# Kernel tuning notes

Hardware: AMD Instinct MI355X
Metric: run time of the kernel (lower is better)

## Reference

```python
import jax, jax.numpy as jnp
import numpy as np

B, C, L = 8, 512, 2048
D = C // 8  # qk projection dim


def setup_inputs() -> dict:
    key = jax.random.key(0)
    ks = jax.random.split(key, 7)
    s = 0.02
    return {
        "x": jax.random.normal(ks[0], (B, C, L), dtype=jnp.float32),
        "data_mask": jnp.zeros((B, L, L), dtype=bool),
        "Wq": jax.random.normal(ks[1], (D, C), dtype=jnp.float32) * s,
        "bq": jnp.zeros((D,), dtype=jnp.float32),
        "Wk": jax.random.normal(ks[2], (D, C), dtype=jnp.float32) * s,
        "bk": jnp.zeros((D,), dtype=jnp.float32),
        "Wv": jax.random.normal(ks[3], (C, C), dtype=jnp.float32) * s,
        "bv": jnp.zeros((C,), dtype=jnp.float32),
    }


def reference(x, data_mask, Wq, bq, Wk, bk, Wv, bv):
    # Conv1d(kernel_size=1) == pointwise linear over channel dim.
    Lx = x.shape[-1]
    q = jnp.einsum("dc,bcl->bld", Wq, x) + bq              # (B, L, D)  == query_conv(x).permute(0,2,1)
    k = jnp.einsum("dc,bcl->bdl", Wk, x) + bk[:, None]     # (B, D, L)
    energy = jnp.einsum("bld,bdm->blm", q, k)              # (B, L, L)
    causal = jnp.triu(jnp.ones((Lx, Lx), dtype=bool), k=1)  # strictly-upper = masked
    mask = causal[None, :, :] | data_mask
    energy = jnp.where(mask, -jnp.inf, energy)
    attention = jax.nn.softmax(energy, axis=-1)            # (B, L, L)
    v = jnp.einsum("oc,bcl->bol", Wv, x) + bv[:, None]     # (B, C, L)
    # out = bmm(proj_value, attention^T): out[b,c,m] = sum_l v[b,c,l] * attention[b,m,l]
    out = jnp.einsum("bcl,bml->bcm", v, attention)         # (B, C, L)
    return out, attention
```

## Files before the change

### kernel.cpp

```cpp
#include <hip/hip_runtime.h>
#include <cstddef>
#include <math.h>

#define B_ 8
#define C_ 512
#define L_ 2048
#define D_ 64

typedef __bf16 bf16x8 __attribute__((ext_vector_type(8)));
typedef __bf16 bf16x4 __attribute__((ext_vector_type(4)));
typedef float f32x4 __attribute__((ext_vector_type(4)));

__device__ __forceinline__ void async_lds16(const void* g, void* l) {
  __builtin_amdgcn_global_load_lds(
      (const __attribute__((address_space(1))) void*)g,
      (__attribute__((address_space(3))) void*)l, 16, 0, 0);
}

__global__ __launch_bounds__(256) void transpose_cvt(const float* __restrict__ x,
                                                     __bf16* __restrict__ xT) {
  __shared__ float t[32][33];
  const int b = blockIdx.z;
  const int l0 = blockIdx.x * 32, c0 = blockIdx.y * 32;
  const int tx = threadIdx.x & 31, ty = threadIdx.x >> 5;
  const float* xb = x + (size_t)b * C_ * L_;
#pragma unroll
  for (int r = 0; r < 4; ++r)
    t[ty + r * 8][tx] = xb[(size_t)(c0 + ty + r * 8) * L_ + l0 + tx];
  __syncthreads();
  __bf16* xTb = xT + (size_t)b * L_ * C_;
#pragma unroll
  for (int r = 0; r < 4; ++r)
    xTb[(size_t)(l0 + ty + r * 8) * C_ + c0 + tx] = (__bf16)t[tx][ty + r * 8];
}

__global__ __launch_bounds__(256) void cvt_bf16(const float* __restrict__ in,
                                                __bf16* __restrict__ out, int n4) {
  const int i = blockIdx.x * 256 + threadIdx.x;
  if (i < n4) {
    float4 v = ((const float4*)in)[i];
    bf16x4 h = {(__bf16)v.x, (__bf16)v.y, (__bf16)v.z, (__bf16)v.w};
    ((bf16x4*)out)[i] = h;
  }
}

template <int TRANS>
__global__ __launch_bounds__(256) void proj_gemm(
    const float* __restrict__ W, const float* __restrict__ bias,
    const float* __restrict__ x, __bf16* __restrict__ out, int M) {
  __shared__ float As[16][68];
  __shared__ float Bs[16][68];
  const int b = blockIdx.z;
  const int m0 = blockIdx.x * 64;
  const int n0 = blockIdx.y * 64;
  const float* xb = x + (size_t)b * C_ * L_;
  const int tid = threadIdx.x;
  const int tm = tid >> 4, tn = tid & 15;
  const int la_m = tid >> 2, la_k = (tid & 3) * 4;
  const int lb_k = tid >> 4, lb_n = (tid & 15) * 4;
  float acc[4][4] = {};
  for (int k0 = 0; k0 < C_; k0 += 16) {
    float4 a4 = *(const float4*)(W + (size_t)(m0 + la_m) * C_ + k0 + la_k);
    As[la_k + 0][la_m] = a4.x;
    As[la_k + 1][la_m] = a4.y;
    As[la_k + 2][la_m] = a4.z;
    As[la_k + 3][la_m] = a4.w;
    float4 b4 = *(const float4*)(xb + (size_t)(k0 + lb_k) * L_ + n0 + lb_n);
    *(float4*)&Bs[lb_k][lb_n] = b4;
    __syncthreads();
#pragma unroll
    for (int k = 0; k < 16; ++k) {
      float4 av = *(const float4*)&As[k][tm * 4];
      float4 bv = *(const float4*)&Bs[k][tn * 4];
      float a[4] = {av.x, av.y, av.z, av.w};
      float bb[4] = {bv.x, bv.y, bv.z, bv.w};
#pragma unroll
      for (int i = 0; i < 4; ++i)
#pragma unroll
        for (int j = 0; j < 4; ++j) acc[i][j] = fmaf(a[i], bb[j], acc[i][j]);
    }
    __syncthreads();
  }
#pragma unroll
  for (int i = 0; i < 4; ++i) {
    const int c = m0 + tm * 4 + i;
    const float bi = bias[c];
#pragma unroll
    for (int j = 0; j < 4; ++j) {
      const int l = n0 + tn * 4 + j;
      const float vv = acc[i][j] + bi;
      if (TRANS)
        out[((size_t)b * L_ + l) * D_ + c] = (__bf16)vv;
      else
        out[((size_t)b * M + c) * L_ + l] = (__bf16)vv;
    }
  }
}

__global__ __launch_bounds__(256) void energy_softmax(
    const __bf16* __restrict__ q, const __bf16* __restrict__ k,
    const unsigned char* __restrict__ mask, float* __restrict__ att) {
  __shared__ __align__(16) __bf16 qs[32 * 64];
  __shared__ __align__(16) __bf16 ks[2][128 * 64];
  __shared__ __align__(16) unsigned char msk[2][32 * 128];
  __shared__ float sums[4][32];
  __shared__ float invs[32];
  const int b = blockIdx.y;
  const int tid = threadIdx.x;
  const int w = tid >> 6, lane = tid & 63;
  const int lm = lane & 15, q8 = lane >> 4;
  const __bf16* qb = q + (size_t)b * L_ * D_;
  const __bf16* kb = k + (size_t)b * L_ * D_;

  for (int half = 0; half < 2; ++half) {
    const int s = half ? (63 - (int)blockIdx.x) : (int)blockIdx.x;
    const int r0 = s * 32;
    const int T = (r0 + 31) / 128 + 1;
    bf16x8 af[2][2];
    float inv[2][4];

    for (int pass = 0; pass < 2; ++pass) {
      __syncthreads();
      if (pass == 0)
        async_lds16(qb + (size_t)r0 * D_ + tid * 8, &qs[w * 512]);
#pragma unroll
      for (int r = 0; r < 4; ++r)
        async_lds16(kb + (size_t)(r * 32) * D_ + tid * 8,
                    &ks[0][r * 2048 + w * 512]);
      async_lds16(mask + (size_t)((size_t)b * L_ + r0 + w * 8 + (lane >> 3)) * L_ +
                      (lane & 7) * 16,
                  &msk[0][w * 1024]);

      float rsum[2][4] = {};
      for (int t = 0; t < T; ++t) {
        const int t0 = t * 128;
        const int buf = t & 1;
        __syncthreads();
        if (pass == 0 && t == 0) {
#pragma unroll
          for (int i = 0; i < 2; ++i)
#pragma unroll
            for (int kk = 0; kk < 2; ++kk)
              af[i][kk] =
                  *(const bf16x8*)&qs[(i * 16 + lm) * 64 + kk * 32 + q8 * 8];
        }
        if (t + 1 < T) {
          const int nt0 = t0 + 128, nb = (t + 1) & 1;
#pragma unroll
          for (int r = 0; r < 4; ++r)
            async_lds16(kb + (size_t)(nt0 + r * 32) * D_ + tid * 8,
                        &ks[nb][r * 2048 + w * 512]);
          async_lds16(mask +
                          (size_t)((size_t)b * L_ + r0 + w * 8 + (lane >> 3)) * L_ +
                          nt0 + (lane & 7) * 16,
                      &msk[nb][w * 1024]);
        }
        f32x4 acc[2][2] = {};
#pragma unroll
        for (int kk = 0; kk < 2; ++kk) {
#pragma unroll
          for (int j = 0; j < 2; ++j) {
            bf16x8 bf = *(const bf16x8*)&ks[buf][(w * 32 + j * 16 + lm) * 64 +
                                                 kk * 32 + q8 * 8];
#pragma unroll
            for (int i = 0; i < 2; ++i)
              acc[i][j] = __builtin_amdgcn_mfma_f32_16x16x32_bf16(
                  af[i][kk], bf, acc[i][j], 0, 0, 0);
          }
        }
#pragma unroll
        for (int i = 0; i < 2; ++i) {
#pragma unroll
          for (int j = 0; j < 2; ++j) {
#pragma unroll
            for (int r = 0; r < 4; ++r) {
              const int lr = i * 16 + q8 * 4 + r;
              const int mcol = w * 32 + j * 16 + lm;
              const int l = r0 + lr, m = t0 + mcol;
              const bool ok = (m <= l) && (msk[buf][lr * 128 + mcol] == 0);
              const float p = ok ? __expf(acc[i][j][r]) : 0.f;
              if (pass == 0)
                rsum[i][r] += p;
              else
                att[((size_t)b * L_ + l) * L_ + m] = p * inv[i][r];
            }
          }
        }
      }
      if (pass == 0) {
#pragma unroll
        for (int i = 0; i < 2; ++i)
#pragma unroll
          for (int r = 0; r < 4; ++r) {
            float v = rsum[i][r];
            v += __shfl_xor(v, 1);
            v += __shfl_xor(v, 2);
            v += __shfl_xor(v, 4);
            v += __shfl_xor(v, 8);
            if (lm == 0) sums[w][i * 16 + q8 * 4 + r] = v;
          }
        __syncthreads();
        if (tid < 32)
          invs[tid] =
              1.f / (sums[0][tid] + sums[1][tid] + sums[2][tid] + sums[3][tid]);
        __syncthreads();
#pragma unroll
        for (int i = 0; i < 2; ++i)
#pragma unroll
          for (int r = 0; r < 4; ++r) inv[i][r] = invs[i * 16 + q8 * 4 + r];
      }
    }
    const float4 z4 = {0.f, 0.f, 0.f, 0.f};
    for (int rr = 0; rr < 32; ++rr) {
      float* arow = att + ((size_t)b * L_ + r0 + rr) * L_;
      for (int c = T * 128 + tid * 4; c < L_; c += 1024)
        *(float4*)&arow[c] = z4;
    }
  }
}

template <int B_CVT, int OUT_BF16, int HAS_BIAS, int TRUNC>
__global__ __launch_bounds__(256) void gemm_bt_mfma(
    const __bf16* __restrict__ A, const void* __restrict__ Bmat,
    const float* __restrict__ bias, void* __restrict__ Cout, int N, int K,
    int lda, int ldb, size_t strideA, size_t strideB, size_t strideC) {
  __shared__ __align__(16) __bf16 Ash[128 * 32];
  __shared__ __align__(16) __bf16 Bsh[128 * 32];
  const int b = blockIdx.z;
  const int m0 = blockIdx.x * 128;
  const int n0 = blockIdx.y * 128;
  const int tid = threadIdx.x;
  const int w = tid >> 6, lane = tid & 63;
  const int wm = (w & 1) * 64, wn = (w >> 1) * 64;
  const int lm = lane & 15, q8 = lane >> 4;

  const __bf16* Ab = A + strideA * b;
  const __bf16* Bh = (const __bf16*)Bmat + strideB * b;
  const float* Bf = (const float*)Bmat + strideB * b;

  f32x4 acc[4][4] = {};
  const int kmax = TRUNC ? (n0 + 128) : K;

  for (int k0 = 0; k0 < kmax; k0 += 32) {
#pragma unroll
    for (int t = 0; t < 2; ++t) {
      const int row_base = (t * 4 + w) * 16;
      const int row = row_base + (lane >> 2);
      const int k8 = lane & 3;
      async_lds16(Ab + (size_t)(m0 + row) * lda + k0 + k8 * 8,
                  &Ash[row_base * 32]);
    }
    if (B_CVT) {
#pragma unroll
      for (int t = 0; t < 4; ++t) {
        const int linear = t * 256 + tid;
        const int row = linear >> 3, k4 = linear & 7;
        float4 v4 = *(const float4*)(Bf + (size_t)(n0 + row) * ldb + k0 + k4 * 4);
        bf16x4 h = {(__bf16)v4.x, (__bf16)v4.y, (__bf16)v4.z, (__bf16)v4.w};
        *(bf16x4*)&Bsh[row * 32 + k4 * 4] = h;
      }
    } else {
#pragma unroll
      for (int t = 0; t < 2; ++t) {
        const int row_base = (t * 4 + w) * 16;
        const int row = row_base + (lane >> 2);
        const int k8 = lane & 3;
        async_lds16(Bh + (size_t)(n0 + row) * ldb + k0 + k8 * 8,
                    &Bsh[row_base * 32]);
      }
    }
    __syncthreads();
    bf16x8 af[4], bfr[4];
#pragma unroll
    for (int i = 0; i < 4; ++i) {
      af[i] = *(const bf16x8*)&Ash[(wm + i * 16 + lm) * 32 + q8 * 8];
      bfr[i] = *(const bf16x8*)&Bsh[(wn + i * 16 + lm) * 32 + q8 * 8];
    }
#pragma unroll
    for (int i = 0; i < 4; ++i)
#pragma unroll
      for (int j = 0; j < 4; ++j)
        acc[i][j] = __builtin_amdgcn_mfma_f32_16x16x32_bf16(af[i], bfr[j],
                                                            acc[i][j], 0, 0, 0);
    __syncthreads();
  }

#pragma unroll
  for (int i = 0; i < 4; ++i) {
#pragma unroll
    for (int j = 0; j < 4; ++j) {
      const int ng = n0 + wn + j * 16 + lm;
#pragma unroll
      for (int r = 0; r < 4; ++r) {
        const int mg = m0 + wm + i * 16 + q8 * 4 + r;
        float val = acc[i][j][r];
        if (HAS_BIAS) val += bias[mg];
        if (OUT_BF16)
          ((__bf16*)Cout)[strideC * b + (size_t)mg * N + ng] = (__bf16)val;
        else
          ((float*)Cout)[strideC * b + (size_t)mg * N + ng] = val;
      }
    }
  }
}

extern "C" void kernel_launch(void* const* d_in, const int* in_sizes, int n_in,
                              void* d_out, int out_size, void* d_ws,
                              size_t ws_size, hipStream_t stream) {
  const float* x = (const float*)d_in[0];
  const unsigned char* dmask = (const unsigned char*)d_in[1];
  const float* Wq = (const float*)d_in[2];
  const float* bq = (const float*)d_in[3];
  const float* Wk = (const float*)d_in[4];
  const float* bk = (const float*)d_in[5];
  const float* Wv = (const float*)d_in[6];
  const float* bv = (const float*)d_in[7];

  float* out = (float*)d_out;
  float* att = out + (size_t)B_ * C_ * L_;

  __bf16* qh = (__bf16*)d_ws;
  __bf16* kh = qh + (size_t)B_ * L_ * D_;
  __bf16* xTh = kh + (size_t)B_ * L_ * D_;
  __bf16* Wvh = xTh + (size_t)B_ * L_ * C_;
  __bf16* vh = Wvh + (size_t)C_ * C_;

  dim3 blk(256);
  transpose_cvt<<<dim3(L_ / 32, C_ / 32, B_), blk, 0, stream>>>(x, xTh);
  cvt_bf16<<<dim3((C_ * C_ / 4 + 255) / 256), blk, 0, stream>>>(Wv, Wvh,
                                                                C_ * C_ / 4);
  proj_gemm<1><<<dim3(1, 32, B_), blk, 0, stream>>>(Wq, bq, x, qh, D_);
  proj_gemm<1><<<dim3(1, 32, B_), blk, 0, stream>>>(Wk, bk, x, kh, D_);
  gemm_bt_mfma<0, 1, 1, 0><<<dim3(C_ / 128, L_ / 128, B_), blk, 0, stream>>>(
      Wvh, xTh, bv, vh, L_, C_, C_, C_, 0, (size_t)L_ * C_, (size_t)C_ * L_);
  energy_softmax<<<dim3(32, B_), blk, 0, stream>>>(qh, kh, dmask, att);
  gemm_bt_mfma<1, 0, 0, 1><<<dim3(C_ / 128, L_ / 128, B_), blk, 0, stream>>>(
      vh, att, nullptr, out, L_, L_, L_, L_, (size_t)C_ * L_, (size_t)L_ * L_,
      (size_t)C_ * L_);
}
```

Baseline: 477.4 us.

## Fuse attention-value product into softmax kernel and use MFMA for Q/K projection

Measured after the change: 418.1 us. 1.14x faster.

```diff
diff --git a/kernel.cpp b/kernel.cpp
--- a/kernel.cpp
+++ b/kernel.cpp
@@ -10,6 +10,8 @@
 typedef __bf16 bf16x8 __attribute__((ext_vector_type(8)));
 typedef __bf16 bf16x4 __attribute__((ext_vector_type(4)));
 typedef float f32x4 __attribute__((ext_vector_type(4)));
+
+#define MFMA16 __builtin_amdgcn_mfma_f32_16x16x32_bf16
 
 __device__ __forceinline__ void async_lds16(const void* g, void* l) {
   __builtin_amdgcn_global_load_lds(
@@ -44,186 +46,28 @@
   }
 }
 
-template <int TRANS>
-__global__ __launch_bounds__(256) void proj_gemm(
-    const float* __restrict__ W, const float* __restrict__ bias,
-    const float* __restrict__ x, __bf16* __restrict__ out, int M) {
-  __shared__ float As[16][68];
-  __shared__ float Bs[16][68];
-  const int b = blockIdx.z;
-  const int m0 = blockIdx.x * 64;
-  const int n0 = blockIdx.y * 64;
-  const float* xb = x + (size_t)b * C_ * L_;
-  const int tid = threadIdx.x;
-  const int tm = tid >> 4, tn = tid & 15;
-  const int la_m = tid >> 2, la_k = (tid & 3) * 4;
-  const int lb_k = tid >> 4, lb_n = (tid & 15) * 4;
-  float acc[4][4] = {};
-  for (int k0 = 0; k0 < C_; k0 += 16) {
-    float4 a4 = *(const float4*)(W + (size_t)(m0 + la_m) * C_ + k0 + la_k);
-    As[la_k + 0][la_m] = a4.x;
-    As[la_k + 1][la_m] = a4.y;
-    As[la_k + 2][la_m] = a4.z;
-    As[la_k + 3][la_m] = a4.w;
-    float4 b4 = *(const float4*)(xb + (size_t)(k0 + lb_k) * L_ + n0 + lb_n);
-    *(float4*)&Bs[lb_k][lb_n] = b4;
-    __syncthreads();
-#pragma unroll
-    for (int k = 0; k < 16; ++k) {
-      float4 av = *(const float4*)&As[k][tm * 4];
-      float4 bv = *(const float4*)&Bs[k][tn * 4];
-      float a[4] = {av.x, av.y, av.z, av.w};
-      float bb[4] = {bv.x, bv.y, bv.z, bv.w};
-#pragma unroll
-      for (int i = 0; i < 4; ++i)
-#pragma unroll
-        for (int j = 0; j < 4; ++j) acc[i][j] = fmaf(a[i], bb[j], acc[i][j]);
-    }
-    __syncthreads();
-  }
-#pragma unroll
-  for (int i = 0; i < 4; ++i) {
-    const int c = m0 + tm * 4 + i;
-    const float bi = bias[c];
-#pragma unroll
-    for (int j = 0; j < 4; ++j) {
-      const int l = n0 + tn * 4 + j;
-      const float vv = acc[i][j] + bi;
-      if (TRANS)
-        out[((size_t)b * L_ + l) * D_ + c] = (__bf16)vv;
-      else
-        out[((size_t)b * M + c) * L_ + l] = (__bf16)vv;
-    }
-  }
-}
-
-__global__ __launch_bounds__(256) void energy_softmax(
-    const __bf16* __restrict__ q, const __bf16* __restrict__ k,
-    const unsigned char* __restrict__ mask, float* __restrict__ att) {
-  __shared__ __align__(16) __bf16 qs[32 * 64];
-  __shared__ __align__(16) __bf16 ks[2][128 * 64];
-  __shared__ __align__(16) unsigned char msk[2][32 * 128];
-  __shared__ float sums[4][32];
-  __shared__ float invs[32];
-  const int b = blockIdx.y;
-  const int tid = threadIdx.x;
-  const int w = tid >> 6, lane = tid & 63;
-  const int lm = lane & 15, q8 = lane >> 4;
-  const __bf16* qb = q + (size_t)b * L_ * D_;
-  const __bf16* kb = k + (size_t)b * L_ * D_;
-
-  for (int half = 0; half < 2; ++half) {
-    const int s = half ? (63 - (int)blockIdx.x) : (int)blockIdx.x;
-    const int r0 = s * 32;
-    const int T = (r0 + 31) / 128 + 1;
-    bf16x8 af[2][2];
-    float inv[2][4];
-
-    for (int pass = 0; pass < 2; ++pass) {
-      __syncthreads();
-      if (pass == 0)
-        async_lds16(qb + (size_t)r0 * D_ + tid * 8, &qs[w * 512]);
-#pragma unroll
-      for (int r = 0; r < 4; ++r)
-        async_lds16(kb + (size_t)(r * 32) * D_ + tid * 8,
-                    &ks[0][r * 2048 + w * 512]);
-      async_lds16(mask + (size_t)((size_t)b * L_ + r0 + w * 8 + (lane >> 3)) * L_ +
-                      (lane & 7) * 16,
-                  &msk[0][w * 1024]);
-
-      float rsum[2][4] = {};
-      for (int t = 0; t < T; ++t) {
-        const int t0 = t * 128;
-        const int buf = t & 1;
-        __syncthreads();
-        if (pass == 0 && t == 0) {
-#pragma unroll
-          for (int i = 0; i < 2; ++i)
-#pragma unroll
-            for (int kk = 0; kk < 2; ++kk)
-              af[i][kk] =
-                  *(const bf16x8*)&qs[(i * 16 + lm) * 64 + kk * 32 + q8 * 8];
-        }
-        if (t + 1 < T) {
-          const int nt0 = t0 + 128, nb = (t + 1) & 1;
-#pragma unroll
-          for (int r = 0; r < 4; ++r)
-            async_lds16(kb + (size_t)(nt0 + r * 32) * D_ + tid * 8,
-                        &ks[nb][r * 2048 + w * 512]);
-          async_lds16(mask +
-                          (size_t)((size_t)b * L_ + r0 + w * 8 + (lane >> 3)) * L_ +
-                          nt0 + (lane & 7) * 16,
-                      &msk[nb][w * 1024]);
-        }
-        f32x4 acc[2][2] = {};
-#pragma unroll
-        for (int kk = 0; kk < 2; ++kk) {
-#pragma unroll
-          for (int j = 0; j < 2; ++j) {
-            bf16x8 bf = *(const bf16x8*)&ks[buf][(w * 32 + j * 16 + lm) * 64 +
-                                                 kk * 32 + q8 * 8];
-#pragma unroll
-            for (int i = 0; i < 2; ++i)
-              acc[i][j] = __builtin_amdgcn_mfma_f32_16x16x32_bf16(
-                  af[i][kk], bf, acc[i][j], 0, 0, 0);
-          }
-        }
-#pragma unroll
-        for (int i = 0; i < 2; ++i) {
-#pragma unroll
-          for (int j = 0; j < 2; ++j) {
-#pragma unroll
-            for (int r = 0; r < 4; ++r) {
-              const int lr = i * 16 + q8 * 4 + r;
-              const int mcol = w * 32 + j * 16 + lm;
-              const int l = r0 + lr, m = t0 + mcol;
-              const bool ok = (m <= l) && (msk[buf][lr * 128 + mcol] == 0);
-              const float p = ok ? __expf(acc[i][j][r]) : 0.f;
-              if (pass == 0)
-                rsum[i][r] += p;
-              else
-                att[((size_t)b * L_ + l) * L_ + m] = p * inv[i][r];
-            }
-          }
-        }
-      }
-      if (pass == 0) {
-#pragma unroll
-        for (int i = 0; i < 2; ++i)
-#pragma unroll
-          for (int r = 0; r < 4; ++r) {
-            float v = rsum[i][r];
-            v += __shfl_xor(v, 1);
-            v += __shfl_xor(v, 2);
-            v += __shfl_xor(v, 4);
-            v += __shfl_xor(v, 8);
-            if (lm == 0) sums[w][i * 16 + q8 * 4 + r] = v;
-          }
-        __syncthreads();
-        if (tid < 32)
-          invs[tid] =
-              1.f / (sums[0][tid] + sums[1][tid] + sums[2][tid] + sums[3][tid]);
-        __syncthreads();
-#pragma unroll
-        for (int i = 0; i < 2; ++i)
-#pragma unroll
-          for (int r = 0; r < 4; ++r) inv[i][r] = invs[i * 16 + q8 * 4 + r];
-      }
-    }
-    const float4 z4 = {0.f, 0.f, 0.f, 0.f};
-    for (int rr = 0; rr < 32; ++rr) {
-      float* arow = att + ((size_t)b * L_ + r0 + rr) * L_;
-      for (int c = T * 128 + tid * 4; c < L_; c += 1024)
-        *(float4*)&arow[c] = z4;
-    }
-  }
-}
-
-template <int B_CVT, int OUT_BF16, int HAS_BIAS, int TRUNC>
+__global__ __launch_bounds__(256) void prep_qk(
+    const float* __restrict__ Wq, const float* __restrict__ Wk,
+    const float* __restrict__ bq, const float* __restrict__ bk,
+    __bf16* __restrict__ Wqk, float* __restrict__ bqk) {
+  const int i = blockIdx.x * 256 + threadIdx.x;
+  const int half = 64 * 512 / 4;
+  const float* src = (i < half) ? Wq : Wk;
+  const int j = (i < half) ? i : i - half;
+  float4 v = ((const float4*)src)[j];
+  bf16x4 h = {(__bf16)v.x, (__bf16)v.y, (__bf16)v.z, (__bf16)v.w};
+  ((bf16x4*)Wqk)[i] = h;
+  if (blockIdx.x == 0 && threadIdx.x < 128)
+    bqk[threadIdx.x] =
+        threadIdx.x < 64 ? bq[threadIdx.x] : bk[threadIdx.x - 64];
+}
+
+template <int QK_MODE>
 __global__ __launch_bounds__(256) void gemm_bt_mfma(
-    const __bf16* __restrict__ A, const void* __restrict__ Bmat,
-    const float* __restrict__ bias, void* __restrict__ Cout, int N, int K,
-    int lda, int ldb, size_t strideA, size_t strideB, size_t strideC) {
+    const __bf16* __restrict__ A, const __bf16* __restrict__ B,
+    const float* __restrict__ bias, __bf16* __restrict__ C0,
+    __bf16* __restrict__ C1, int N, int K, int lda, int ldb, size_t strideA,
+    size_t strideB, size_t strideC) {
   __shared__ __align__(16) __bf16 Ash[128 * 32];
   __shared__ __align__(16) __bf16 Bsh[128 * 32];
   const int b = blockIdx.z;
@@ -233,55 +77,35 @@
   const int w = tid >> 6, lane = tid & 63;
   const int wm = (w & 1) * 64, wn = (w >> 1) * 64;
   const int lm = lane & 15, q8 = lane >> 4;
+  const int srow = lane >> 2;
+  const int sk8 = (lane & 3) ^ ((lane >> 3) & 3);
 
   const __bf16* Ab = A + strideA * b;
-  const __bf16* Bh = (const __bf16*)Bmat + strideB * b;
-  const float* Bf = (const float*)Bmat + strideB * b;
-
+  const __bf16* Bb = B + strideB * b;
   f32x4 acc[4][4] = {};
-  const int kmax = TRUNC ? (n0 + 128) : K;
-
-  for (int k0 = 0; k0 < kmax; k0 += 32) {
+
+  for (int k0 = 0; k0 < K; k0 += 32) {
 #pragma unroll
     for (int t = 0; t < 2; ++t) {
-      const int row_base = (t * 4 + w) * 16;
-      const int row = row_base + (lane >> 2);
-      const int k8 = lane & 3;
-      async_lds16(Ab + (size_t)(m0 + row) * lda + k0 + k8 * 8,
-                  &Ash[row_base * 32]);
-    }
-    if (B_CVT) {
-#pragma unroll
-      for (int t = 0; t < 4; ++t) {
-        const int linear = t * 256 + tid;
-        const int row = linear >> 3, k4 = linear & 7;
-        float4 v4 = *(const float4*)(Bf + (size_t)(n0 + row) * ldb + k0 + k4 * 4);
-        bf16x4 h = {(__bf16)v4.x, (__bf16)v4.y, (__bf16)v4.z, (__bf16)v4.w};
-        *(bf16x4*)&Bsh[row * 32 + k4 * 4] = h;
-      }
-    } else {
-#pragma unroll
-      for (int t = 0; t < 2; ++t) {
-        const int row_base = (t * 4 + w) * 16;
-        const int row = row_base + (lane >> 2);
-        const int k8 = lane & 3;
-        async_lds16(Bh + (size_t)(n0 + row) * ldb + k0 + k8 * 8,
-                    &Bsh[row_base * 32]);
-      }
+      const int rb = (t * 4 + w) * 16;
+      async_lds16(Ab + (size_t)(m0 + rb + srow) * lda + k0 + sk8 * 8,
+                  &Ash[rb * 32]);
+      async_lds16(Bb + (size_t)(n0 + rb + srow) * ldb + k0 + sk8 * 8,
+                  &Bsh[rb * 32]);
     }
     __syncthreads();
-    bf16x8 af[4], bfr[4];
+    const int swz = (q8 ^ ((lm >> 1) & 3)) * 8;
+    bf16x8 afr[4], bfr[4];
 #pragma unroll
     for (int i = 0; i < 4; ++i) {
-      af[i] = *(const bf16x8*)&Ash[(wm + i * 16 + lm) * 32 + q8 * 8];
-      bfr[i] = *(const bf16x8*)&Bsh[(wn + i * 16 + lm) * 32 + q8 * 8];
+      afr[i] = *(const bf16x8*)&Ash[(wm + i * 16 + lm) * 32 + swz];
+      bfr[i] = *(const bf16x8*)&Bsh[(wn + i * 16 + lm) * 32 + swz];
     }
 #pragma unroll
     for (int i = 0; i < 4; ++i)
 #pragma unroll
       for (int j = 0; j < 4; ++j)
-        acc[i][j] = __builtin_amdgcn_mfma_f32_16x16x32_bf16(af[i], bfr[j],
-                                                            acc[i][j], 0, 0, 0);
+        acc[i][j] = MFMA16(afr[i], bfr[j], acc[i][j], 0, 0, 0);
     __syncthreads();
   }
 
@@ -290,17 +114,182 @@
 #pragma unroll
     for (int j = 0; j < 4; ++j) {
       const int ng = n0 + wn + j * 16 + lm;
-#pragma unroll
-      for (int r = 0; r < 4; ++r) {
-        const int mg = m0 + wm + i * 16 + q8 * 4 + r;
-        float val = acc[i][j][r];
-        if (HAS_BIAS) val += bias[mg];
-        if (OUT_BF16)
-          ((__bf16*)Cout)[strideC * b + (size_t)mg * N + ng] = (__bf16)val;
+      const int mgb = wm + i * 16 + q8 * 4;
+      if (QK_MODE) {
+        bf16x4 h;
+#pragma unroll
+        for (int r = 0; r < 4; ++r) h[r] = (__bf16)(acc[i][j][r] + bias[mgb + r]);
+        if (mgb < 64)
+          *(bf16x4*)&C0[((size_t)b * L_ + ng) * 64 + mgb] = h;
         else
-          ((float*)Cout)[strideC * b + (size_t)mg * N + ng] = val;
-      }
-    }
+          *(bf16x4*)&C1[((size_t)b * L_ + ng) * 64 + mgb - 64] = h;
+      } else {
+#pragma unroll
+        for (int r = 0; r < 4; ++r) {
+          const int mg = m0 + mgb + r;
+          C0[strideC * b + (size_t)mg * N + ng] =
+              (__bf16)(acc[i][j][r] + bias[mg]);
+        }
+      }
+    }
+  }
+}
+
+__global__ __launch_bounds__(256) void attn_fused(
+    const __bf16* __restrict__ q, const __bf16* __restrict__ k,
+    const __bf16* __restrict__ v, const unsigned char* __restrict__ mask,
+    float* __restrict__ att, float* __restrict__ out) {
+  __shared__ __align__(16) __bf16 qs[32 * 64];
+  __shared__ __align__(16) __bf16 ks[2][128 * 64];
+  __shared__ __align__(16) unsigned char msk[2][32 * 128];
+  __shared__ __align__(16) __bf16 Ps[32 * 136];
+  __shared__ float sums[4][32];
+  __shared__ float invs[32];
+  const int b = blockIdx.y;
+  const int s = (b < 4) ? (int)blockIdx.x : 63 - (int)blockIdx.x;
+  const int r0 = s * 32;
+  const int T = (r0 + 31) / 128 + 1;
+  const int tid = threadIdx.x;
+  const int w = tid >> 6, lane = tid & 63;
+  const int lm = lane & 15, q8 = lane >> 4;
+  const __bf16* qb = q + (size_t)b * L_ * D_;
+  const __bf16* kb = k + (size_t)b * L_ * D_;
+  const __bf16* vb = v + (size_t)b * C_ * L_;
+  const int krow = lane >> 3;
+  const int kk8 = (lane & 7) ^ ((lane >> 3) & 7);
+
+  bf16x8 af[2][2];
+  float inv[2][4];
+  f32x4 accO[2][8] = {};
+
+  for (int pass = 0; pass < 2; ++pass) {
+    __syncthreads();
+    if (pass == 0)
+      async_lds16(qb + (size_t)r0 * D_ + tid * 8, &qs[w * 512]);
+#pragma unroll
+    for (int r = 0; r < 4; ++r)
+      async_lds16(kb + (size_t)(r * 32 + w * 8 + krow) * 64 + kk8 * 8,
+                  &ks[0][(r * 32 + w * 8) * 64]);
+    async_lds16(mask + (size_t)((size_t)b * L_ + r0 + w * 8 + krow) * L_ +
+                    (lane & 7) * 16,
+                &msk[0][w * 1024]);
+
+    float rsum[2][4] = {};
+    for (int t = 0; t < T; ++t) {
+      const int t0 = t * 128;
+      const int buf = t & 1;
+      __syncthreads();
+      if (pass == 0 && t == 0) {
+#pragma unroll
+        for (int i = 0; i < 2; ++i)
+#pragma unroll
+          for (int kk = 0; kk < 2; ++kk)
+            af[i][kk] =
+                *(const bf16x8*)&qs[(i * 16 + lm) * 64 + kk * 32 + q8 * 8];
+      }
+      if (t + 1 < T) {
+        const int nt0 = t0 + 128, nb = (t + 1) & 1;
+#pragma unroll
+        for (int r = 0; r < 4; ++r)
+          async_lds16(kb + (size_t)(nt0 + r * 32 + w * 8 + krow) * 64 + kk8 * 8,
+                      &ks[nb][(r * 32 + w * 8) * 64]);
+        async_lds16(mask + (size_t)((size_t)b * L_ + r0 + w * 8 + krow) * L_ +
+                        nt0 + (lane & 7) * 16,
+                    &msk[nb][w * 1024]);
+      }
+      f32x4 acc[2][2] = {};
+#pragma unroll
+      for (int kk = 0; kk < 2; ++kk) {
+#pragma unroll
+        for (int j = 0; j < 2; ++j) {
+          const int n = w * 32 + j * 16 + lm;
+          const int k8i = kk * 4 + q8;
+          bf16x8 bf =
+              *(const bf16x8*)&ks[buf][n * 64 + ((k8i ^ (n & 7)) * 8)];
+#pragma unroll
+          for (int i = 0; i < 2; ++i)
+            acc[i][j] = MFMA16(af[i][kk], bf, acc[i][j], 0, 0, 0);
+        }
+      }
+#pragma unroll
+      for (int i = 0; i < 2; ++i)
+#pragma unroll
+        for (int j = 0; j < 2; ++j)
+#pragma unroll
+          for (int r = 0; r < 4; ++r) {
+            const int lr = i * 16 + q8 * 4 + r;
+            const int mcol = w * 32 + j * 16 + lm;
+            const int l = r0 + lr, m = t0 + mcol;
+            const bool ok = (m <= l) && (msk[buf][lr * 128 + mcol] == 0);
+            const float p = ok ? __expf(acc[i][j][r]) : 0.f;
+            if (pass == 0) {
+              rsum[i][r] += p;
+            } else {
+              att[((size_t)b * L_ + l) * L_ + m] = p * inv[i][r];
+              Ps[lr * 136 + mcol] = (__bf16)p;
+            }
+          }
+      if (pass == 1) {
+        __syncthreads();
+#pragma unroll
+        for (int kk = 0; kk < 4; ++kk) {
+          bf16x8 pa[2];
+#pragma unroll
+          for (int i = 0; i < 2; ++i)
+            pa[i] = *(const bf16x8*)&Ps[(i * 16 + lm) * 136 + kk * 32 + q8 * 8];
+#pragma unroll
+          for (int cf = 0; cf < 8; ++cf) {
+            const int c = w * 128 + cf * 16 + lm;
+            bf16x8 bv =
+                *(const bf16x8*)(vb + (size_t)c * L_ + t0 + kk * 32 + q8 * 8);
+#pragma unroll
+            for (int i = 0; i < 2; ++i)
+              accO[i][cf] = MFMA16(pa[i], bv, accO[i][cf], 0, 0, 0);
+          }
+        }
+      }
+    }
+    if (pass == 0) {
+#pragma unroll
+      for (int i = 0; i < 2; ++i)
+#pragma unroll
+        for (int r = 0; r < 4; ++r) {
+          float vv = rsum[i][r];
+          vv += __shfl_xor(vv, 1);
+          vv += __shfl_xor(vv, 2);
+          vv += __shfl_xor(vv, 4);
+          vv += __shfl_xor(vv, 8);
+          if (lm == 0) sums[w][i * 16 + q8 * 4 + r] = vv;
+        }
+      __syncthreads();
+      if (tid < 32)
+        invs[tid] =
+            1.f / (sums[0][tid] + sums[1][tid] + sums[2][tid] + sums[3][tid]);
+      __syncthreads();
+#pragma unroll
+      for (int i = 0; i < 2; ++i)
+#pragma unroll
+        for (int r = 0; r < 4; ++r) inv[i][r] = invs[i * 16 + q8 * 4 + r];
+    }
+  }
+
+#pragma unroll
+  for (int i = 0; i < 2; ++i)
+#pragma unroll
+    for (int cf = 0; cf < 8; ++cf) {
+      const int c = w * 128 + cf * 16 + lm;
+      float4 o;
+      o.x = accO[i][cf][0] * inv[i][0];
+      o.y = accO[i][cf][1] * inv[i][1];
+      o.z = accO[i][cf][2] * inv[i][2];
+      o.w = accO[i][cf][3] * inv[i][3];
+      *(float4*)(out + ((size_t)b * C_ + c) * L_ + r0 + i * 16 + q8 * 4) = o;
+    }
+
+  const float4 z4 = {0.f, 0.f, 0.f, 0.f};
+  for (int rr = 0; rr < 32; ++rr) {
+    float* arow = att + ((size_t)b * L_ + r0 + rr) * L_;
+    for (int c = T * 128 + tid * 4; c < L_; c += 1024) *(float4*)&arow[c] = z4;
   }
 }
 
@@ -324,17 +313,17 @@
   __bf16* xTh = kh + (size_t)B_ * L_ * D_;
   __bf16* Wvh = xTh + (size_t)B_ * L_ * C_;
   __bf16* vh = Wvh + (size_t)C_ * C_;
+  __bf16* Wqk = vh + (size_t)B_ * C_ * L_;
+  float* bqk = (float*)(Wqk + (size_t)128 * C_);
 
   dim3 blk(256);
   transpose_cvt<<<dim3(L_ / 32, C_ / 32, B_), blk, 0, stream>>>(x, xTh);
-  cvt_bf16<<<dim3((C_ * C_ / 4 + 255) / 256), blk, 0, stream>>>(Wv, Wvh,
-                                                                C_ * C_ / 4);
-  proj_gemm<1><<<dim3(1, 32, B_), blk, 0, stream>>>(Wq, bq, x, qh, D_);
-  proj_gemm<1><<<dim3(1, 32, B_), blk, 0, stream>>>(Wk, bk, x, kh, D_);
-  gemm_bt_mfma<0, 1, 1, 0><<<dim3(C_ / 128, L_ / 128, B_), blk, 0, stream>>>(
-      Wvh, xTh, bv, vh, L_, C_, C_, C_, 0, (size_t)L_ * C_, (size_t)C_ * L_);
-  energy_softmax<<<dim3(32, B_), blk, 0, stream>>>(qh, kh, dmask, att);
-  gemm_bt_mfma<1, 0, 0, 1><<<dim3(C_ / 128, L_ / 128, B_), blk, 0, stream>>>(
-      vh, att, nullptr, out, L_, L_, L_, L_, (size_t)C_ * L_, (size_t)L_ * L_,
+  cvt_bf16<<<dim3(C_ * C_ / 4 / 256), blk, 0, stream>>>(Wv, Wvh, C_ * C_ / 4);
+  prep_qk<<<dim3(64), blk, 0, stream>>>(Wq, Wk, bq, bk, Wqk, bqk);
+  gemm_bt_mfma<1><<<dim3(1, L_ / 128, B_), blk, 0, stream>>>(
+      Wqk, xTh, bqk, qh, kh, L_, C_, C_, C_, 0, (size_t)L_ * C_, 0);
+  gemm_bt_mfma<0><<<dim3(C_ / 128, L_ / 128, B_), blk, 0, stream>>>(
+      Wvh, xTh, bv, vh, nullptr, L_, C_, C_, C_, 0, (size_t)L_ * C_,
       (size_t)C_ * L_);
-}
+  attn_fused<<<dim3(64, B_), blk, 0, stream>>>(qh, kh, vh, dmask, att, out);
+}
```
